# Kernel optimization log

Measured on AMD Instinct MI355X. Metric: run time of the kernel, lower is better.

Reference implementation:

```python
import jax, jax.numpy as jnp
import numpy as np

D_MODEL = 512
NUM_HEADS = 8
DEPTH = D_MODEL // NUM_HEADS


def setup_inputs() -> dict:
    key = jax.random.key(0)
    kx, kq, kk, kv, ko = jax.random.split(key, 5)
    scale = 1.0 / np.sqrt(D_MODEL)
    return {
        "x": jax.random.normal(kx, (4, 2048, D_MODEL), dtype=jnp.float32),
        "W_q": jax.random.normal(kq, (D_MODEL, D_MODEL), dtype=jnp.float32) * scale,
        "W_k": jax.random.normal(kk, (D_MODEL, D_MODEL), dtype=jnp.float32) * scale,
        "W_v": jax.random.normal(kv, (D_MODEL, D_MODEL), dtype=jnp.float32) * scale,
        "W_o": jax.random.normal(ko, (D_MODEL, D_MODEL), dtype=jnp.float32) * scale,
    }


def reference(x, W_q, W_k, W_v, W_o):
    B, S, _ = x.shape
    # nn.Linear with weight W: y = x @ W.T
    def split_heads(t):
        return t.reshape(B, S, NUM_HEADS, DEPTH).transpose(0, 2, 1, 3)  # [B,H,S,D]
    Q = split_heads(x @ W_q.T)
    K = split_heads(x @ W_k.T)
    V = split_heads(x @ W_v.T)
    b = -jnp.log(jnp.asarray(S, dtype=jnp.float32))  # -log(seq_len) bias
    inv_sqrt_dk = 1.0 / jnp.sqrt(jnp.asarray(DEPTH, dtype=jnp.float32))
    qk = jnp.einsum('bhqd,bhkd->bhqk', Q, K) * inv_sqrt_dk
    attn = jax.nn.sigmoid(qk + b)  # non-softmax sigmoid attention
    out = jnp.einsum('bhqk,bhkd->bhqd', attn, V)
    out = out.transpose(0, 2, 1, 3).reshape(B, S, D_MODEL)
    return out @ W_o.T
```

## Files before the change

### kernel.cpp

```cpp
#include <hip/hip_runtime.h>
#include <stdint.h>

typedef _Float16 f16x8 __attribute__((ext_vector_type(8)));
typedef _Float16 f16x4 __attribute__((ext_vector_type(4)));
typedef __fp16 h16x2 __attribute__((ext_vector_type(2)));
typedef float f32x4 __attribute__((ext_vector_type(4)));
typedef float f32x16 __attribute__((ext_vector_type(16)));

#define SEQ 2048
#define NHEADS 8

#define GLOAD_LDS16(gp, lp)                                                        \
  __builtin_amdgcn_global_load_lds(                                                \
      (const __attribute__((address_space(1))) void*)(uintptr_t)(const void*)(gp), \
      (__attribute__((address_space(3))) void*)(uintptr_t)(void*)(lp), 16, 0, 0)

__device__ __forceinline__ void barrier_lds() {
  __builtin_amdgcn_s_waitcnt(0xc07f);
  __builtin_amdgcn_s_barrier();
}

__device__ __forceinline__ f16x4 pack4(float a, float b, float c, float d) {
  h16x2 lo = __builtin_amdgcn_cvt_pkrtz(a, b);
  h16x2 hi = __builtin_amdgcn_cvt_pkrtz(c, d);
  f16x4 o;
  o.x = (_Float16)lo.x; o.y = (_Float16)lo.y;
  o.z = (_Float16)hi.x; o.w = (_Float16)hi.y;
  return o;
}

__global__ void cvt_all_kernel(const float* __restrict__ x, const float* __restrict__ wq,
                               const float* __restrict__ wk, const float* __restrict__ wv,
                               const float* __restrict__ wo, _Float16* __restrict__ xh,
                               _Float16* __restrict__ wh) {
  int i = blockIdx.x * 256 + threadIdx.x;
  const float* src;
  _Float16* dst;
  int off;
  if (i < 1048576) {
    src = x; dst = xh; off = i;
  } else {
    int j = i - 1048576;
    int sel = j >> 16;
    off = j & 65535;
    src = (sel == 0) ? wq : (sel == 1) ? wk : (sel == 2) ? wv : wo;
    dst = wh + (size_t)sel * 262144;
  }
  float4 v = ((const float4*)src)[off];
  ((f16x4*)dst)[off] = pack4(v.x, v.y, v.z, v.w);
}

__device__ __forceinline__ void gemm_tile_bt(const _Float16* __restrict__ A,
                                             const _Float16* __restrict__ B,
                                             int m0, int n0,
                                             _Float16* lds,
                                             f32x4 (&acc)[4][4]) {
  const int tid = threadIdx.x;
  const int w = tid >> 6, lane = tid & 63;
  const int wr = w >> 1, wc = w & 1;
  const int lrow = lane & 15, q = lane >> 4;
  const int snb = w * 32 + (lane >> 3);
  const int scb = lane & 7;

#pragma unroll
  for (int i = 0; i < 4; ++i)
#pragma unroll
    for (int j = 0; j < 4; ++j)
#pragma unroll
      for (int r = 0; r < 4; ++r) acc[i][j][r] = 0.f;

#pragma unroll
  for (int t = 0; t < 4; ++t) {
    int n = snb + t * 8;
    int cbg = scb ^ (n & 7);
    GLOAD_LDS16(A + (size_t)(m0 + n) * 512 + cbg * 8, lds + (w * 32 + t * 8) * 64);
    GLOAD_LDS16(B + (size_t)(n0 + n) * 512 + cbg * 8, lds + 8192 + (w * 32 + t * 8) * 64);
  }

  for (int kt = 0; kt < 8; ++kt) {
    __syncthreads();
    if (kt < 7) {
      _Float16* nb = lds + ((kt + 1) & 1) * 16384;
#pragma unroll
      for (int t = 0; t < 4; ++t) {
        int n = snb + t * 8;
        int cbg = scb ^ (n & 7);
        GLOAD_LDS16(A + (size_t)(m0 + n) * 512 + (kt + 1) * 64 + cbg * 8, nb + (w * 32 + t * 8) * 64);
        GLOAD_LDS16(B + (size_t)(n0 + n) * 512 + (kt + 1) * 64 + cbg * 8, nb + 8192 + (w * 32 + t * 8) * 64);
      }
    }
    _Float16* As = lds + (kt & 1) * 16384;
    _Float16* Bs = As + 8192;

    f16x8 af[4][2], bfr[4][2];
#pragma unroll
    for (int i = 0; i < 4; ++i) {
      int m = wr * 64 + i * 16 + lrow;
#pragma unroll
      for (int kk = 0; kk < 2; ++kk) {
        int cb = (kk * 4 + q) ^ (m & 7);
        af[i][kk] = *(const f16x8*)(As + m * 64 + cb * 8);
      }
    }
#pragma unroll
    for (int j = 0; j < 4; ++j) {
      int n = wc * 64 + j * 16 + lrow;
#pragma unroll
      for (int kk = 0; kk < 2; ++kk) {
        int cb = (kk * 4 + q) ^ (n & 7);
        bfr[j][kk] = *(const f16x8*)(Bs + n * 64 + cb * 8);
      }
    }
#pragma unroll
    for (int i = 0; i < 4; ++i)
#pragma unroll
      for (int j = 0; j < 4; ++j) {
        acc[i][j] = __builtin_amdgcn_mfma_f32_16x16x32_f16(af[i][0], bfr[j][0], acc[i][j], 0, 0, 0);
        acc[i][j] = __builtin_amdgcn_mfma_f32_16x16x32_f16(af[i][1], bfr[j][1], acc[i][j], 0, 0, 0);
      }
  }
}

__global__ __launch_bounds__(256, 2) void qkv_kernel(
    const _Float16* __restrict__ xb, const _Float16* __restrict__ Wq,
    const _Float16* __restrict__ Wk, const _Float16* __restrict__ Wv,
    _Float16* __restrict__ Qo, _Float16* __restrict__ Ko, _Float16* __restrict__ Vto) {
  __shared__ _Float16 pool[32768];
  const int z = blockIdx.z;
  f32x4 acc[4][4];
  const int tid = threadIdx.x, w = tid >> 6, lane = tid & 63;
  const int wr = w >> 1, wc = w & 1, lcol = lane & 15, q = lane >> 4;

  if (z < 2) {
    const int m0 = blockIdx.y * 128;
    const int n0 = blockIdx.x * 128;
    gemm_tile_bt((z == 0) ? Wq : Wk, xb, m0, n0, pool, acc);
    _Float16* outp = (z == 0) ? Qo : Ko;
    __syncthreads();
#pragma unroll
    for (int i = 0; i < 4; ++i) {
      int cl = wr * 64 + i * 16 + q * 4;
#pragma unroll
      for (int j = 0; j < 4; ++j) {
        int s = wc * 64 + j * 16 + lcol;
        *(f16x4*)(pool + s * 136 + cl) =
            pack4(acc[i][j][0], acc[i][j][1], acc[i][j][2], acc[i][j][3]);
      }
    }
    __syncthreads();
#pragma unroll
    for (int it = 0; it < 16; ++it) {
      int srow = it * 8 + (tid >> 5);
      int ch = tid & 31;
      f16x4 v = *(const f16x4*)(pool + srow * 136 + ch * 4);
      *(f16x4*)(outp + (size_t)(n0 + srow) * 512 + m0 + ch * 4) = v;
    }
  } else {
    const int m0 = blockIdx.x * 128;
    const int n0 = blockIdx.y * 128;
    gemm_tile_bt(xb, Wv, m0, n0, pool, acc);
    const int bb = m0 >> 11, sl0 = m0 & 2047;
    __syncthreads();
#pragma unroll
    for (int i = 0; i < 4; ++i) {
      int s0 = wr * 64 + i * 16 + q * 4;
#pragma unroll
      for (int j = 0; j < 4; ++j) {
        int c = wc * 64 + j * 16 + lcol;
        *(f16x4*)(pool + c * 136 + s0) =
            pack4(acc[i][j][0], acc[i][j][1], acc[i][j][2], acc[i][j][3]);
      }
    }
    __syncthreads();
#pragma unroll
    for (int it = 0; it < 16; ++it) {
      int crow = it * 8 + (tid >> 5);
      int ch = tid & 31;
      int cg = n0 + crow, h = cg >> 6, d = cg & 63;
      f16x4 v = *(const f16x4*)(pool + crow * 136 + ch * 4);
      *(f16x4*)(Vto + ((size_t)((bb * NHEADS + h) * 64 + d)) * SEQ + sl0 + ch * 4) = v;
    }
  }
}

__global__ __launch_bounds__(256, 2) void attn_kernel(
    const _Float16* __restrict__ Qw, const _Float16* __restrict__ Kw,
    const _Float16* __restrict__ Vtw, _Float16* __restrict__ Ow) {
  __shared__ _Float16 lds[32768];

  const int tid = threadIdx.x, w = tid >> 6, lane = tid & 63;
  const int q31 = lane & 31, hi = lane >> 5;

  const int L = blockIdx.x;
  const int xcd = L & 7, slot = L >> 3;
  const int bh = xcd * 4 + (slot >> 4), qt = slot & 15;
  const int b = bh >> 3, h = bh & 7;
  const int q0 = qt * 128;

  const _Float16* Qp = Qw + ((size_t)(b * SEQ + q0)) * 512 + h * 64;
  const _Float16* Kp = Kw + ((size_t)b * SEQ) * 512 + h * 64;
  const _Float16* Vp = Vtw + (size_t)bh * 64 * SEQ;

  const int snb = w * 32 + (lane >> 3), scb = lane & 7;
  const int vnb = w * 16 + (lane >> 4), vcb = lane & 15;

  _Float16* Qs = lds;
#pragma unroll
  for (int t = 0; t < 4; ++t) {
    int n = snb + t * 8;
    int cbg = scb ^ (n & 7);
    GLOAD_LDS16(Qp + (size_t)n * 512 + cbg * 8, Qs + (w * 32 + t * 8) * 64);
  }
  __syncthreads();

  f16x8 qb[4];
  const int qrow = w * 32 + q31;
#pragma unroll
  for (int s = 0; s < 4; ++s) {
    int cb = (s * 2 + hi) ^ (qrow & 7);
    qb[s] = *(const f16x8*)(Qs + qrow * 64 + cb * 8);
  }
  barrier_lds();

#pragma unroll
  for (int t = 0; t < 4; ++t) {
    int n = snb + t * 8;
    int cbg = scb ^ (n & 7);
    GLOAD_LDS16(Kp + (size_t)n * 512 + cbg * 8, lds + (w * 32 + t * 8) * 64);
  }
#pragma unroll
  for (int t = 0; t < 4; ++t) {
    int nv = vnb + t * 4;
    int cbg = vcb ^ (nv & 15);
    GLOAD_LDS16(Vp + (size_t)nv * SEQ + cbg * 8, lds + 8192 + (w * 16 + t * 4) * 128);
  }

  f32x16 oacc[2];
  f32x16 z16;
#pragma unroll
  for (int r = 0; r < 16; ++r) { z16[r] = 0.f; oacc[0][r] = 0.f; oacc[1][r] = 0.f; }

  const int klp = (q31 & 3) | ((q31 & 4) << 1) | ((q31 & 8) >> 1) | (q31 & 16);

  const float c1 = 0.18033688011112042f;

  for (int kt = 0; kt < 16; ++kt) {
    __syncthreads();
    if (kt < 15) {
      _Float16* nb = lds + ((kt + 1) & 1) * 16384;
#pragma unroll
      for (int t = 0; t < 4; ++t) {
        int n = snb + t * 8;
        int cbg = scb ^ (n & 7);
        GLOAD_LDS16(Kp + (size_t)((kt + 1) * 128 + n) * 512 + cbg * 8, nb + (w * 32 + t * 8) * 64);
      }
#pragma unroll
      for (int t = 0; t < 4; ++t) {
        int nv = vnb + t * 4;
        int cbg = vcb ^ (nv & 15);
        GLOAD_LDS16(Vp + (size_t)nv * SEQ + (kt + 1) * 128 + cbg * 8, nb + 8192 + (w * 16 + t * 4) * 128);
      }
    }
    _Float16* Ksc = lds + (kt & 1) * 16384;
    _Float16* Vtsc = Ksc + 8192;

#pragma unroll
    for (int m = 0; m < 4; ++m) {
      const int krow = m * 32 + klp;
      f16x8 ka[4];
#pragma unroll
      for (int s = 0; s < 4; ++s) {
        int cb = (s * 2 + hi) ^ (krow & 7);
        ka[s] = *(const f16x8*)(Ksc + krow * 64 + cb * 8);
      }
      f16x8 vb[2][2];
#pragma unroll
      for (int ww = 0; ww < 2; ++ww)
#pragma unroll
        for (int t = 0; t < 2; ++t) {
          int drow = t * 32 + q31;
          int g = m * 4 + ww * 2 + hi;
          int cb = g ^ (drow & 15);
          vb[ww][t] = *(const f16x8*)(Vtsc + drow * 128 + cb * 8);
        }

      f32x16 sacc = __builtin_amdgcn_mfma_f32_32x32x16_f16(ka[0], qb[0], z16, 0, 0, 0);
      sacc = __builtin_amdgcn_mfma_f32_32x32x16_f16(ka[1], qb[1], sacc, 0, 0, 0);
      sacc = __builtin_amdgcn_mfma_f32_32x32x16_f16(ka[2], qb[2], sacc, 0, 0, 0);
      sacc = __builtin_amdgcn_mfma_f32_32x32x16_f16(ka[3], qb[3], sacc, 0, 0, 0);

      float p[16];
#pragma unroll
      for (int r = 0; r < 16; ++r) {
        float wp = __builtin_amdgcn_exp2f(__builtin_fmaf(sacc[r], c1, -1.0f));
        float e = wp * 0.0009765625f;
        p[r] = __builtin_fmaf(wp, __builtin_fmaf(e, e, -e), wp);
      }

      f16x8 pa[2];
#pragma unroll
      for (int ww = 0; ww < 2; ++ww) {
        h16x2 a0 = __builtin_amdgcn_cvt_pkrtz(p[8 * ww + 0], p[8 * ww + 1]);
        h16x2 a1 = __builtin_amdgcn_cvt_pkrtz(p[8 * ww + 2], p[8 * ww + 3]);
        h16x2 a2 = __builtin_amdgcn_cvt_pkrtz(p[8 * ww + 4], p[8 * ww + 5]);
        h16x2 a3 = __builtin_amdgcn_cvt_pkrtz(p[8 * ww + 6], p[8 * ww + 7]);
        pa[ww][0] = (_Float16)a0.x; pa[ww][1] = (_Float16)a0.y;
        pa[ww][2] = (_Float16)a1.x; pa[ww][3] = (_Float16)a1.y;
        pa[ww][4] = (_Float16)a2.x; pa[ww][5] = (_Float16)a2.y;
        pa[ww][6] = (_Float16)a3.x; pa[ww][7] = (_Float16)a3.y;
      }

      oacc[0] = __builtin_amdgcn_mfma_f32_32x32x16_f16(pa[0], vb[0][0], oacc[0], 0, 0, 0);
      oacc[1] = __builtin_amdgcn_mfma_f32_32x32x16_f16(pa[0], vb[0][1], oacc[1], 0, 0, 0);
      oacc[0] = __builtin_amdgcn_mfma_f32_32x32x16_f16(pa[1], vb[1][0], oacc[0], 0, 0, 0);
      oacc[1] = __builtin_amdgcn_mfma_f32_32x32x16_f16(pa[1], vb[1][1], oacc[1], 0, 0, 0);
    }
  }

  barrier_lds();
  _Float16* Ob = lds;
#pragma unroll
  for (int t = 0; t < 2; ++t) {
#pragma unroll
    for (int r = 0; r < 16; ++r) {
      int row = w * 32 + (r & 3) + ((r >> 2) << 3) + hi * 4;
      int d = t * 32 + q31;
      Ob[row * 72 + d] = (_Float16)(oacc[t][r] * 0.0009765625f);
    }
  }
  barrier_lds();
#pragma unroll
  for (int it = 0; it < 8; ++it) {
    int row = it * 16 + (tid >> 4);
    int ch = tid & 15;
    f16x4 v = *(const f16x4*)(Ob + row * 72 + ch * 4);
    *(f16x4*)(Ow + (size_t)(b * SEQ + q0 + row) * 512 + h * 64 + ch * 4) = v;
  }
}

__global__ __launch_bounds__(256, 2) void oproj_kernel(
    const _Float16* __restrict__ A, const _Float16* __restrict__ Wo,
    float* __restrict__ out) {
  __shared__ _Float16 pool[32768];
  const int m0 = blockIdx.x * 128, n0 = blockIdx.y * 128;
  f32x4 acc[4][4];
  gemm_tile_bt(A, Wo, m0, n0, pool, acc);

  const int tid = threadIdx.x, w = tid >> 6, lane = tid & 63;
  const int wr = w >> 1, wc = w & 1, lcol = lane & 15, q = lane >> 4;
#pragma unroll
  for (int i = 0; i < 4; ++i) {
    int gm0 = m0 + wr * 64 + i * 16 + q * 4;
#pragma unroll
    for (int j = 0; j < 4; ++j) {
      int gn = n0 + wc * 64 + j * 16 + lcol;
#pragma unroll
      for (int r = 0; r < 4; ++r)
        out[(size_t)(gm0 + r) * 512 + gn] = acc[i][j][r];
    }
  }
}

extern "C" void kernel_launch(void* const* d_in, const int* in_sizes, int n_in,
                              void* d_out, int out_size, void* d_ws, size_t ws_size,
                              hipStream_t stream) {
  const float* x = (const float*)d_in[0];
  const float* Wq = (const float*)d_in[1];
  const float* Wk = (const float*)d_in[2];
  const float* Wv = (const float*)d_in[3];
  const float* Wo = (const float*)d_in[4];
  float* out = (float*)d_out;
  char* ws = (char*)d_ws;

  _Float16* xh = (_Float16*)(ws + 0);
  _Float16* wh = (_Float16*)(ws + 8388608);
  _Float16* Qw = (_Float16*)(ws + 10485760);
  _Float16* Kw = (_Float16*)(ws + 18874368);
  _Float16* Vtw = (_Float16*)(ws + 27262976);
  _Float16* Ow = (_Float16*)(ws + 35651584);

  _Float16* wqh = wh;
  _Float16* wkh = wh + 262144;
  _Float16* wvh = wh + 524288;
  _Float16* woh = wh + 786432;

  cvt_all_kernel<<<5120, 256, 0, stream>>>(x, Wq, Wk, Wv, Wo, xh, wh);
  qkv_kernel<<<dim3(64, 4, 3), 256, 0, stream>>>(xh, wqh, wkh, wvh, Qw, Kw, Vtw);
  attn_kernel<<<512, 256, 0, stream>>>(Qw, Kw, Vtw, Ow);
  oproj_kernel<<<dim3(64, 4), 256, 0, stream>>>(Ow, woh, out);
}
```

Baseline: 149.5 us.

## Double-buffer LDS fragment loads in attention loop, add MFMA priority hints

The attention inner loop now loads K and V register fragments one window ahead, ping-ponging between two register sets so LDS reads overlap the MFMA and exp work of the previous window. It also raises wave priority with s_setprio around the MFMA groups and issues the Q, K and V prologue loads together, with Q in the upper LDS region, so one barrier replaces two. Global load addresses are precomputed as byte offsets and advanced by pointer bumps to cut index arithmetic. The extra fragment registers could raise VGPR pressure at the 2-blocks-per-CU launch bound.

```diff
diff --git a/kernel.cpp b/kernel.cpp
--- a/kernel.cpp
+++ b/kernel.cpp
@@ -183,6 +183,66 @@
   }
 }
 
+__device__ __forceinline__ void load_win(const _Float16* Ksc, const _Float16* Vtsc,
+                                         int m, int klp, int hi, int q31,
+                                         f16x8 (&ka)[4], f16x8 (&vb)[2][2]) {
+  const int krow = m * 32 + klp;
+#pragma unroll
+  for (int s = 0; s < 4; ++s) {
+    int cb = (s * 2 + hi) ^ (krow & 7);
+    ka[s] = *(const f16x8*)(Ksc + krow * 64 + cb * 8);
+  }
+#pragma unroll
+  for (int ww = 0; ww < 2; ++ww)
+#pragma unroll
+    for (int t = 0; t < 2; ++t) {
+      int drow = t * 32 + q31;
+      int g = m * 4 + ww * 2 + hi;
+      int cb = g ^ (drow & 15);
+      vb[ww][t] = *(const f16x8*)(Vtsc + drow * 128 + cb * 8);
+    }
+}
+
+__device__ __forceinline__ void attn_window(const f16x8 (&ka)[4], const f16x8 (&vb)[2][2],
+                                            const f16x8 (&qb)[4], const f32x16& z16,
+                                            f32x16& o0, f32x16& o1) {
+  const float c1 = 0.18033688011112042f;
+  __builtin_amdgcn_s_setprio(1);
+  f32x16 sacc = __builtin_amdgcn_mfma_f32_32x32x16_f16(ka[0], qb[0], z16, 0, 0, 0);
+  sacc = __builtin_amdgcn_mfma_f32_32x32x16_f16(ka[1], qb[1], sacc, 0, 0, 0);
+  sacc = __builtin_amdgcn_mfma_f32_32x32x16_f16(ka[2], qb[2], sacc, 0, 0, 0);
+  sacc = __builtin_amdgcn_mfma_f32_32x32x16_f16(ka[3], qb[3], sacc, 0, 0, 0);
+  __builtin_amdgcn_s_setprio(0);
+
+  float p[16];
+#pragma unroll
+  for (int r = 0; r < 16; ++r) {
+    float wp = __builtin_amdgcn_exp2f(__builtin_fmaf(sacc[r], c1, -1.0f));
+    float e = wp * 0.0009765625f;
+    p[r] = __builtin_fmaf(wp, __builtin_fmaf(e, e, -e), wp);
+  }
+
+  f16x8 pa[2];
+#pragma unroll
+  for (int ww = 0; ww < 2; ++ww) {
+    h16x2 a0 = __builtin_amdgcn_cvt_pkrtz(p[8 * ww + 0], p[8 * ww + 1]);
+    h16x2 a1 = __builtin_amdgcn_cvt_pkrtz(p[8 * ww + 2], p[8 * ww + 3]);
+    h16x2 a2 = __builtin_amdgcn_cvt_pkrtz(p[8 * ww + 4], p[8 * ww + 5]);
+    h16x2 a3 = __builtin_amdgcn_cvt_pkrtz(p[8 * ww + 6], p[8 * ww + 7]);
+    pa[ww][0] = (_Float16)a0.x; pa[ww][1] = (_Float16)a0.y;
+    pa[ww][2] = (_Float16)a1.x; pa[ww][3] = (_Float16)a1.y;
+    pa[ww][4] = (_Float16)a2.x; pa[ww][5] = (_Float16)a2.y;
+    pa[ww][6] = (_Float16)a3.x; pa[ww][7] = (_Float16)a3.y;
+  }
+
+  __builtin_amdgcn_s_setprio(1);
+  o0 = __builtin_amdgcn_mfma_f32_32x32x16_f16(pa[0], vb[0][0], o0, 0, 0, 0);
+  o1 = __builtin_amdgcn_mfma_f32_32x32x16_f16(pa[0], vb[0][1], o1, 0, 0, 0);
+  o0 = __builtin_amdgcn_mfma_f32_32x32x16_f16(pa[1], vb[1][0], o0, 0, 0, 0);
+  o1 = __builtin_amdgcn_mfma_f32_32x32x16_f16(pa[1], vb[1][1], o1, 0, 0, 0);
+  __builtin_amdgcn_s_setprio(0);
+}
+
 __global__ __launch_bounds__(256, 2) void attn_kernel(
     const _Float16* __restrict__ Qw, const _Float16* __restrict__ Kw,
     const _Float16* __restrict__ Vtw, _Float16* __restrict__ Ow) {
@@ -204,13 +264,26 @@
   const int snb = w * 32 + (lane >> 3), scb = lane & 7;
   const int vnb = w * 16 + (lane >> 4), vcb = lane & 15;
 
-  _Float16* Qs = lds;
+  int koff[4], voff[4];
+  const int kcb = scb ^ (snb & 7);
 #pragma unroll
   for (int t = 0; t < 4; ++t) {
-    int n = snb + t * 8;
-    int cbg = scb ^ (n & 7);
-    GLOAD_LDS16(Qp + (size_t)n * 512 + cbg * 8, Qs + (w * 32 + t * 8) * 64);
-  }
+    koff[t] = snb * 1024 + t * 8192 + kcb * 16;
+    int nv = vnb + t * 4;
+    voff[t] = nv * 4096 + (vcb ^ (nv & 15)) * 16;
+  }
+  const char* kgb = (const char*)Kp;
+  const char* vgb = (const char*)Vp;
+
+  _Float16* Qs = lds + 16384;
+#pragma unroll
+  for (int t = 0; t < 4; ++t) GLOAD_LDS16((const char*)Qp + koff[t], Qs + (w * 32 + t * 8) * 64);
+#pragma unroll
+  for (int t = 0; t < 4; ++t) GLOAD_LDS16(kgb + koff[t], lds + (w * 32 + t * 8) * 64);
+#pragma unroll
+  for (int t = 0; t < 4; ++t) GLOAD_LDS16(vgb + voff[t], lds + 8192 + (w * 16 + t * 4) * 128);
+  kgb += 131072;
+  vgb += 256;
   __syncthreads();
 
   f16x8 qb[4];
@@ -220,20 +293,6 @@
     int cb = (s * 2 + hi) ^ (qrow & 7);
     qb[s] = *(const f16x8*)(Qs + qrow * 64 + cb * 8);
   }
-  barrier_lds();
-
-#pragma unroll
-  for (int t = 0; t < 4; ++t) {
-    int n = snb + t * 8;
-    int cbg = scb ^ (n & 7);
-    GLOAD_LDS16(Kp + (size_t)n * 512 + cbg * 8, lds + (w * 32 + t * 8) * 64);
-  }
-#pragma unroll
-  for (int t = 0; t < 4; ++t) {
-    int nv = vnb + t * 4;
-    int cbg = vcb ^ (nv & 15);
-    GLOAD_LDS16(Vp + (size_t)nv * SEQ + cbg * 8, lds + 8192 + (w * 16 + t * 4) * 128);
-  }
 
   f32x16 oacc[2];
   f32x16 z16;
@@ -242,79 +301,29 @@
 
   const int klp = (q31 & 3) | ((q31 & 4) << 1) | ((q31 & 8) >> 1) | (q31 & 16);
 
-  const float c1 = 0.18033688011112042f;
-
   for (int kt = 0; kt < 16; ++kt) {
     __syncthreads();
     if (kt < 15) {
       _Float16* nb = lds + ((kt + 1) & 1) * 16384;
 #pragma unroll
-      for (int t = 0; t < 4; ++t) {
-        int n = snb + t * 8;
-        int cbg = scb ^ (n & 7);
-        GLOAD_LDS16(Kp + (size_t)((kt + 1) * 128 + n) * 512 + cbg * 8, nb + (w * 32 + t * 8) * 64);
-      }
-#pragma unroll
-      for (int t = 0; t < 4; ++t) {
-        int nv = vnb + t * 4;
-        int cbg = vcb ^ (nv & 15);
-        GLOAD_LDS16(Vp + (size_t)nv * SEQ + (kt + 1) * 128 + cbg * 8, nb + 8192 + (w * 16 + t * 4) * 128);
-      }
-    }
-    _Float16* Ksc = lds + (kt & 1) * 16384;
-    _Float16* Vtsc = Ksc + 8192;
-
-#pragma unroll
-    for (int m = 0; m < 4; ++m) {
-      const int krow = m * 32 + klp;
-      f16x8 ka[4];
-#pragma unroll
-      for (int s = 0; s < 4; ++s) {
-        int cb = (s * 2 + hi) ^ (krow & 7);
-        ka[s] = *(const f16x8*)(Ksc + krow * 64 + cb * 8);
-      }
-      f16x8 vb[2][2];
-#pragma unroll
-      for (int ww = 0; ww < 2; ++ww)
-#pragma unroll
-        for (int t = 0; t < 2; ++t) {
-          int drow = t * 32 + q31;
-          int g = m * 4 + ww * 2 + hi;
-          int cb = g ^ (drow & 15);
-          vb[ww][t] = *(const f16x8*)(Vtsc + drow * 128 + cb * 8);
-        }
-
-      f32x16 sacc = __builtin_amdgcn_mfma_f32_32x32x16_f16(ka[0], qb[0], z16, 0, 0, 0);
-      sacc = __builtin_amdgcn_mfma_f32_32x32x16_f16(ka[1], qb[1], sacc, 0, 0, 0);
-      sacc = __builtin_amdgcn_mfma_f32_32x32x16_f16(ka[2], qb[2], sacc, 0, 0, 0);
-      sacc = __builtin_amdgcn_mfma_f32_32x32x16_f16(ka[3], qb[3], sacc, 0, 0, 0);
-
-      float p[16];
-#pragma unroll
-      for (int r = 0; r < 16; ++r) {
-        float wp = __builtin_amdgcn_exp2f(__builtin_fmaf(sacc[r], c1, -1.0f));
-        float e = wp * 0.0009765625f;
-        p[r] = __builtin_fmaf(wp, __builtin_fmaf(e, e, -e), wp);
-      }
-
-      f16x8 pa[2];
-#pragma unroll
-      for (int ww = 0; ww < 2; ++ww) {
-        h16x2 a0 = __builtin_amdgcn_cvt_pkrtz(p[8 * ww + 0], p[8 * ww + 1]);
-        h16x2 a1 = __builtin_amdgcn_cvt_pkrtz(p[8 * ww + 2], p[8 * ww + 3]);
-        h16x2 a2 = __builtin_amdgcn_cvt_pkrtz(p[8 * ww + 4], p[8 * ww + 5]);
-        h16x2 a3 = __builtin_amdgcn_cvt_pkrtz(p[8 * ww + 6], p[8 * ww + 7]);
-        pa[ww][0] = (_Float16)a0.x; pa[ww][1] = (_Float16)a0.y;
-        pa[ww][2] = (_Float16)a1.x; pa[ww][3] = (_Float16)a1.y;
-        pa[ww][4] = (_Float16)a2.x; pa[ww][5] = (_Float16)a2.y;
-        pa[ww][6] = (_Float16)a3.x; pa[ww][7] = (_Float16)a3.y;
-      }
-
-      oacc[0] = __builtin_amdgcn_mfma_f32_32x32x16_f16(pa[0], vb[0][0], oacc[0], 0, 0, 0);
-      oacc[1] = __builtin_amdgcn_mfma_f32_32x32x16_f16(pa[0], vb[0][1], oacc[1], 0, 0, 0);
-      oacc[0] = __builtin_amdgcn_mfma_f32_32x32x16_f16(pa[1], vb[1][0], oacc[0], 0, 0, 0);
-      oacc[1] = __builtin_amdgcn_mfma_f32_32x32x16_f16(pa[1], vb[1][1], oacc[1], 0, 0, 0);
-    }
+      for (int t = 0; t < 4; ++t) GLOAD_LDS16(kgb + koff[t], nb + (w * 32 + t * 8) * 64);
+#pragma unroll
+      for (int t = 0; t < 4; ++t) GLOAD_LDS16(vgb + voff[t], nb + 8192 + (w * 16 + t * 4) * 128);
+      kgb += 131072;
+      vgb += 256;
+    }
+    const _Float16* Ksc = lds + (kt & 1) * 16384;
+    const _Float16* Vtsc = Ksc + 8192;
+
+    f16x8 kaA[4], kaB[4], vbA[2][2], vbB[2][2];
+    load_win(Ksc, Vtsc, 0, klp, hi, q31, kaA, vbA);
+    load_win(Ksc, Vtsc, 1, klp, hi, q31, kaB, vbB);
+    attn_window(kaA, vbA, qb, z16, oacc[0], oacc[1]);
+    load_win(Ksc, Vtsc, 2, klp, hi, q31, kaA, vbA);
+    attn_window(kaB, vbB, qb, z16, oacc[0], oacc[1]);
+    load_win(Ksc, Vtsc, 3, klp, hi, q31, kaB, vbB);
+    attn_window(kaA, vbA, qb, z16, oacc[0], oacc[1]);
+    attn_window(kaB, vbB, qb, z16, oacc[0], oacc[1]);
   }
 
   barrier_lds();
```

After: 153.9 us. 1.03x slower.
